# Performance work log

Measured on AMD Instinct MI355X. Metric: run time of the kernel, lower is better.

Reference implementation:

```python
import jax, jax.numpy as jnp
import numpy as np

B = 256
# (Cin, Cout, K, Hout) for each of the 6 deformable conv layers; input is 33x33
_LAYERS = [(1, 16, 3, 31), (16, 32, 3, 29), (32, 16, 5, 25), (16, 16, 7, 19), (16, 8, 5, 15), (8, 4, 3, 13)]


def setup_inputs() -> dict:
    key = jax.random.key(0)
    ks = jax.random.split(key, 24)
    inp = {"x": jax.random.normal(ks[0], (B, 1, 33, 33), dtype=jnp.float32)}
    for i, (ci, co, k, ho) in enumerate(_LAYERS):
        inp[f"off{i+1}"] = jax.random.normal(ks[1 + i], (1, 2 * k * k, ho, ho), dtype=jnp.float32)
        inp[f"w{i+1}"] = jax.random.normal(ks[7 + i], (co, ci, k, k), dtype=jnp.float32) / float(np.sqrt(ci * k * k))
        inp[f"b{i+1}"] = jnp.zeros((co,), jnp.float32)
    inp["w7"] = jax.random.normal(ks[13], (13 * 13 * 4, 256), dtype=jnp.float32) / 26.0
    inp["b7"] = jnp.zeros((256,), jnp.float32)
    inp["w8"] = jax.random.normal(ks[14], (256, 10), dtype=jnp.float32) / 16.0
    inp["b8"] = jnp.zeros((10,), jnp.float32)
    inp["perm"] = jnp.arange(13 * 13, dtype=jnp.int32)  # fixed spatial permutation (perm_6.ordenar)
    return inp


def _deform_conv(x, offset, weight, bias):
    # torchvision DeformConv2d, stride=1, padding=0, fixed offsets shared across batch.
    Bn, Cin, H, W = x.shape
    Cout, _, K, _ = weight.shape
    Ho, Wo = offset.shape[-2], offset.shape[-1]
    K2 = K * K
    off = offset[0].reshape(K2, 2, Ho, Wo)  # channel layout: [2k]=dy, [2k+1]=dx
    ky, kx = jnp.meshgrid(jnp.arange(K), jnp.arange(K), indexing='ij')
    py = jnp.arange(Ho, dtype=x.dtype)[None, :, None] + ky.reshape(-1, 1, 1) + off[:, 0]  # [K2,Ho,Wo]
    px = jnp.arange(Wo, dtype=x.dtype)[None, None, :] + kx.reshape(-1, 1, 1) + off[:, 1]
    y0f = jnp.floor(py); x0f = jnp.floor(px)
    wy = py - y0f; wx = px - x0f
    y0 = y0f.astype(jnp.int32); x0 = x0f.astype(jnp.int32)
    xf = x.reshape(Bn, Cin, H * W)

    def gather(yi, xi):
        valid = ((yi >= 0) & (yi < H) & (xi >= 0) & (xi < W)).astype(x.dtype)
        idx = (jnp.clip(yi, 0, H - 1) * W + jnp.clip(xi, 0, W - 1)).reshape(-1)
        v = xf[:, :, idx].reshape(Bn, Cin, K2, Ho, Wo)
        return v * valid[None, None]

    s = (gather(y0, x0) * ((1 - wy) * (1 - wx))[None, None]
         + gather(y0, x0 + 1) * ((1 - wy) * wx)[None, None]
         + gather(y0 + 1, x0) * (wy * (1 - wx))[None, None]
         + gather(y0 + 1, x0 + 1) * (wy * wx)[None, None])  # [B,Cin,K2,Ho,Wo]
    out = jnp.einsum('bckhw,ock->bohw', s, weight.reshape(Cout, Cin, K2))
    return out + bias[None, :, None, None]


def reference(x, off1, off2, off3, off4, off5, off6,
              w1, b1, w2, b2, w3, b3, w4, b4, w5, b5, w6, b6,
              w7, b7, w8, b8, perm):
    offs = (off1, off2, off3, off4, off5, off6)
    ws = (w1, w2, w3, w4, w5, w6)
    bs = (b1, b2, b3, b4, b5, b6)
    for off, w, b in zip(offs, ws, bs):
        x = jax.nn.relu(_deform_conv(x, off, w, b))
    Bn = x.shape[0]
    x = x.reshape(Bn, 4, 13 * 13)[:, :, perm].reshape(Bn, -1)  # perm_6.ordenar as spatial permutation
    h = jax.nn.relu(x @ w7 + b7)
    return h @ w8 + b8
```

## Files before the change

### kernel.cpp

```cpp
#include <hip/hip_runtime.h>

template<int N> struct IC { static constexpr int val = N; };

struct WtArgs { const float* src[6]; int co[6], ci[6], k2[6], dstoff[6]; };

__global__ __launch_bounds__(256)
void transpose_weights(WtArgs a, float* __restrict__ dst0)
{
    const int L = blockIdx.x;
    const float* __restrict__ s = a.src[L];
    float* __restrict__ d = dst0 + a.dstoff[L];
    const int co = a.co[L], ci = a.ci[L], k2 = a.k2[L];
    const int n = co * ci * k2;
    for (int i = threadIdx.x; i < n; i += 256) {
        int k = i % k2;
        int c = (i / k2) % ci;
        int o = i / (k2 * ci);
        d[(k * ci + c) * co + o] = s[i];
    }
}

struct MetaArgs { const float* off[6]; int P[6], K[6], WO[6], H[6], W[6], base[6]; };

__global__ __launch_bounds__(256)
void build_meta(MetaArgs a, float* __restrict__ meta0)
{
    const int L = blockIdx.y;
    const float* __restrict__ off = a.off[L];
    const int P = a.P[L], K = a.K[L], WOv = a.WO[L], H = a.H[L], Wv = a.W[L];
    const int N = P * K * K;
    float* __restrict__ m = meta0 + (size_t)a.base[L] * 8;
    for (int e = blockIdx.x * 256 + threadIdx.x; e < N; e += gridDim.x * 256) {
        const int k = e / P, p = e - k * P;
        const int ho = p / WOv, wo = p - ho * WOv;
        const int ky = k / K, kx = k - ky * K;
        const float dy = off[(2 * k)     * P + p];
        const float dx = off[(2 * k + 1) * P + p];
        const float py = (float)(ho + ky) + dy;
        const float px = (float)(wo + kx) + dx;
        const float y0f = floorf(py), x0f = floorf(px);
        const float wy = py - y0f, wx = px - x0f;
        const int y0 = (int)y0f, x0 = (int)x0f;
        const int y1 = y0 + 1,  x1 = x0 + 1;
        const bool vy0 = ((unsigned)y0 < (unsigned)H);
        const bool vy1 = ((unsigned)y1 < (unsigned)H);
        const bool vx0 = ((unsigned)x0 < (unsigned)Wv);
        const bool vx1 = ((unsigned)x1 < (unsigned)Wv);
        const int cy0 = min(max(y0, 0), H - 1) * Wv;
        const int cy1 = min(max(y1, 0), H - 1) * Wv;
        const int cx0 = min(max(x0, 0), Wv - 1);
        const int cx1 = min(max(x1, 0), Wv - 1);
        int4 mi;
        mi.x = cy0 + cx0; mi.y = cy0 + cx1; mi.z = cy1 + cx0; mi.w = cy1 + cx1;
        float4 mw;
        mw.x = (vy0 && vx0) ? (1.f - wy) * (1.f - wx) : 0.f;
        mw.y = (vy0 && vx1) ? (1.f - wy) * wx         : 0.f;
        mw.z = (vy1 && vx0) ? wy * (1.f - wx)         : 0.f;
        mw.w = (vy1 && vx1) ? wy * wx                 : 0.f;
        *(int4*)(m + (size_t)e * 8)       = mi;
        *(float4*)(m + (size_t)e * 8 + 4) = mw;
    }
}

template<int CIN, int CINW, int COUT, int K, int H, int W, int HO, int WO,
         int S, int KSEG, int NT, int NCOMB, bool SPLITOUT, bool MET,
         int NSL = 1, int CINL = 0>
__global__ __launch_bounds__(NT)
void deform_lds(const float* __restrict__ x0, const float* __restrict__ x1,
                const float* __restrict__ x2, const float* __restrict__ off,
                const float* __restrict__ meta, const float* __restrict__ wT,
                const float* __restrict__ bias, float* __restrict__ y,
                size_t pstride)
{
    constexpr int K2 = K * K, HW = H * W, P = HO * WO;
    constexpr int PW = ((P + 63) / 64) * 64;
    constexpr int KLEN = (K2 + KSEG - 1) / KSEG;
    constexpr int PSTR = (COUT % 2 == 0) ? COUT + 1 : COUT;
    static_assert(NT >= KSEG * PW, "NT too small for KSEG*PW");

    __shared__ __align__(16) float simg[HW * S];
    __shared__ float part[(KSEG > 1) ? (KSEG - 1) * P * PSTR : 1];

    const int tid = threadIdx.x;
    const int b   = blockIdx.x;
    const int h   = SPLITOUT ? blockIdx.y : 0;

    const size_t xoff = (size_t)b * CINW * HW + (SPLITOUT ? (size_t)h * CIN * HW : 0);
    const float* xb  = x0 + xoff;
    const float* xb1 = (NCOMB >= 2) ? (x1 + xoff) : nullptr;
    const float* xb2 = (NCOMB == 3) ? (x2 + xoff) : nullptr;
    for (int i = tid; i < CIN * HW; i += NT) {
        int c = i / HW, hw = i - c * HW;
        bool ok = true;
        if constexpr (SPLITOUT) ok = (h * CIN + c < CINW);
        float v = 0.f;
        if (ok) {
            v = xb[i];
            if constexpr (NCOMB >= 2) v += xb1[i];
            if constexpr (NCOMB == 3) v += xb2[i];
            if constexpr (NCOMB >= 2) v = fmaxf(v, 0.f);
        }
        simg[hw * S + c] = v;
    }
    __syncthreads();

    const int g  = tid / PW;
    const int p  = tid - g * PW;
    const int pc = (p < P) ? p : (P - 1);
    const bool active = (p < P);

    float acc[COUT];
#pragma unroll
    for (int o = 0; o < COUT; ++o) acc[o] = 0.f;

    if (g < KSEG) {
        if (g == 0 && (!SPLITOUT || h == 0)) {
#pragma unroll
            for (int o = 0; o < COUT; ++o) acc[o] = bias[o];
        }
        const int ho = pc / WO, wo = pc - ho * WO;
        const int kb = g * KLEN;

        auto run = [&](auto nc4tag) {
            constexpr int NC4 = decltype(nc4tag)::val;

            auto fma_block = [&](int i00, int i01, int i10, int i11,
                                 float w00, float w01, float w10, float w11,
                                 int kku) {
                const float* __restrict__ r00 = simg + i00 * S;
                const float* __restrict__ r01 = simg + i01 * S;
                const float* __restrict__ r10 = simg + i10 * S;
                const float* __restrict__ r11 = simg + i11 * S;
                const float* __restrict__ wk = wT + kku * (CINW * COUT)
                                             + (SPLITOUT ? h * (CIN * COUT) : 0);
                if constexpr (CIN % 4 == 0) {
#pragma unroll
                    for (int c4 = 0; c4 < NC4; ++c4) {
                        const float4 v00 = *(const float4*)(r00 + c4 * 4);
                        const float4 v01 = *(const float4*)(r01 + c4 * 4);
                        const float4 v10 = *(const float4*)(r10 + c4 * 4);
                        const float4 v11 = *(const float4*)(r11 + c4 * 4);
                        float4 sa;
                        sa.x = fmaf(w00, v00.x, fmaf(w01, v01.x, fmaf(w10, v10.x, w11 * v11.x)));
                        sa.y = fmaf(w00, v00.y, fmaf(w01, v01.y, fmaf(w10, v10.y, w11 * v11.y)));
                        sa.z = fmaf(w00, v00.z, fmaf(w01, v01.z, fmaf(w10, v10.z, w11 * v11.z)));
                        sa.w = fmaf(w00, v00.w, fmaf(w01, v01.w, fmaf(w10, v10.w, w11 * v11.w)));
                        const float* __restrict__ wc = wk + (c4 * 4) * COUT;
#pragma unroll
                        for (int o = 0; o < COUT; ++o) acc[o] = fmaf(wc[o], sa.x, acc[o]);
#pragma unroll
                        for (int o = 0; o < COUT; ++o) acc[o] = fmaf(wc[COUT + o], sa.y, acc[o]);
#pragma unroll
                        for (int o = 0; o < COUT; ++o) acc[o] = fmaf(wc[2 * COUT + o], sa.z, acc[o]);
#pragma unroll
                        for (int o = 0; o < COUT; ++o) acc[o] = fmaf(wc[3 * COUT + o], sa.w, acc[o]);
                    }
                } else {
#pragma unroll
                    for (int c = 0; c < CIN; ++c) {
                        float sa = fmaf(w00, r00[c], fmaf(w01, r01[c],
                                   fmaf(w10, r10[c], w11 * r11[c])));
#pragma unroll
                        for (int o = 0; o < COUT; ++o)
                            acc[o] = fmaf(wk[c * COUT + o], sa, acc[o]);
                    }
                }
            };

            if constexpr (MET) {
                const int kf = (kb < K2) ? kb : (K2 - 1);
                int4   nmi = *(const int4*)  (meta + (size_t)(kf * P + pc) * 8);
                float4 nmw = *(const float4*)(meta + (size_t)(kf * P + pc) * 8 + 4);

#pragma unroll 1
                for (int j = 0; j < KLEN; ++j) {
                    const int k  = kb + j;
                    const int kk = (k < K2) ? k : (K2 - 1);
                    const int4   mi  = nmi;
                    const float4 mwv = nmw;
                    const int kn = (k + 1 < K2) ? (k + 1) : (K2 - 1);
                    nmi = *(const int4*)  (meta + (size_t)(kn * P + pc) * 8);
                    nmw = *(const float4*)(meta + (size_t)(kn * P + pc) * 8 + 4);

                    float w00 = mwv.x, w01 = mwv.y, w10 = mwv.z, w11 = mwv.w;
                    if constexpr (K2 % KSEG != 0) {
                        const float kv = (k < K2) ? 1.f : 0.f;
                        w00 *= kv; w01 *= kv; w10 *= kv; w11 *= kv;
                    }
                    const int kku = __builtin_amdgcn_readfirstlane(kk);
                    fma_block(mi.x, mi.y, mi.z, mi.w, w00, w01, w10, w11, kku);
                }
            } else {
                const int kf = (kb < K2) ? kb : (K2 - 1);
                float ndy = off[(2 * kf)     * P + pc];
                float ndx = off[(2 * kf + 1) * P + pc];

#pragma unroll 1
                for (int j = 0; j < KLEN; ++j) {
                    const int k  = kb + j;
                    const int kk = (k < K2) ? k : (K2 - 1);
                    const float dy = ndy, dx = ndx;
                    const int kn = (k + 1 < K2) ? (k + 1) : (K2 - 1);
                    ndy = off[(2 * kn)     * P + pc];
                    ndx = off[(2 * kn + 1) * P + pc];

                    const int ky = kk / K, kx = kk - ky * K;
                    const float py = (float)(ho + ky) + dy;
                    const float px = (float)(wo + kx) + dx;
                    const float y0f = floorf(py), x0f = floorf(px);
                    const float wy = py - y0f, wx = px - x0f;
                    const int y0 = (int)y0f, x0 = (int)x0f;
                    const int y1 = y0 + 1,  x1i = x0 + 1;
                    const bool vy0 = ((unsigned)y0  < (unsigned)H);
                    const bool vy1 = ((unsigned)y1  < (unsigned)H);
                    const bool vx0 = ((unsigned)x0  < (unsigned)W);
                    const bool vx1 = ((unsigned)x1i < (unsigned)W);
                    const int cy0 = min(max(y0, 0), H - 1) * W;
                    const int cy1 = min(max(y1, 0), H - 1) * W;
                    const int cx0 = min(max(x0, 0), W - 1);
                    const int cx1 = min(max(x1i, 0), W - 1);
                    float w00 = (vy0 && vx0) ? (1.f - wy) * (1.f - wx) : 0.f;
                    float w01 = (vy0 && vx1) ? (1.f - wy) * wx         : 0.f;
                    float w10 = (vy1 && vx0) ? wy * (1.f - wx)         : 0.f;
                    float w11 = (vy1 && vx1) ? wy * wx                 : 0.f;
                    if constexpr (K2 % KSEG != 0) {
                        const float kv = (k < K2) ? 1.f : 0.f;
                        w00 *= kv; w01 *= kv; w10 *= kv; w11 *= kv;
                    }
                    const int kku = __builtin_amdgcn_readfirstlane(kk);
                    fma_block(cy0 + cx0, cy0 + cx1, cy1 + cx0, cy1 + cx1,
                              w00, w01, w10, w11, kku);
                }
            }
        };

        if constexpr (SPLITOUT && CINL > 0) {
            if (h == NSL - 1) run(IC<(CINL + 3) / 4>{});
            else              run(IC<(CIN + 3) / 4>{});
        } else {
            run(IC<(CIN + 3) / 4>{});
        }

        if (g > 0 && active) {
#pragma unroll
            for (int o = 0; o < COUT; ++o)
                part[(g - 1) * (P * PSTR) + p * PSTR + o] = acc[o];
        }
    }

    if constexpr (KSEG > 1) __syncthreads();

    if (g == 0 && active) {
        if constexpr (KSEG > 1) {
#pragma unroll
            for (int gg = 1; gg < KSEG; ++gg)
#pragma unroll
                for (int o = 0; o < COUT; ++o)
                    acc[o] += part[(gg - 1) * (P * PSTR) + p * PSTR + o];
        }
        float* yb = y + (SPLITOUT ? (size_t)h * pstride : 0) + (size_t)b * COUT * P;
#pragma unroll
        for (int o = 0; o < COUT; ++o)
            yb[o * P + p] = SPLITOUT ? acc[o] : fmaxf(acc[o], 0.f);
    }
}

__global__ __launch_bounds__(256)
void fc_head(const float* __restrict__ x6, const float* __restrict__ w7,
             const float* __restrict__ b7, const float* __restrict__ w8,
             const float* __restrict__ b8, const int* __restrict__ perm,
             float* __restrict__ out)
{
    constexpr int F = 676;
    __shared__ float sx[F];
    __shared__ float sh[256];

    const int tid = threadIdx.x;
    const int b   = blockIdx.x;

    for (int i = tid; i < F; i += 256) {
        int c = i / 169, p = i - c * 169;
        sx[i] = x6[(size_t)b * F + c * 169 + perm[p]];
    }
    __syncthreads();

    float acc = b7[tid];
#pragma unroll 4
    for (int i = 0; i < F; ++i)
        acc = fmaf(sx[i], w7[i * 256 + tid], acc);
    sh[tid] = fmaxf(acc, 0.f);
    __syncthreads();

    if (tid < 10) {
        float a = b8[tid];
#pragma unroll 8
        for (int j = 0; j < 256; ++j)
            a = fmaf(sh[j], w8[j * 10 + tid], a);
        out[(size_t)b * 10 + tid] = a;
    }
}

extern "C" void kernel_launch(void* const* d_in, const int* in_sizes, int n_in,
                              void* d_out, int out_size, void* d_ws, size_t ws_size,
                              hipStream_t stream)
{
    const float* x    = (const float*)d_in[0];
    const float* off1 = (const float*)d_in[1];
    const float* w1   = (const float*)d_in[2];
    const float* b1   = (const float*)d_in[3];
    const float* off2 = (const float*)d_in[4];
    const float* w2   = (const float*)d_in[5];
    const float* b2   = (const float*)d_in[6];
    const float* off3 = (const float*)d_in[7];
    const float* w3   = (const float*)d_in[8];
    const float* b3   = (const float*)d_in[9];
    const float* off4 = (const float*)d_in[10];
    const float* w4   = (const float*)d_in[11];
    const float* b4   = (const float*)d_in[12];
    const float* off5 = (const float*)d_in[13];
    const float* w5   = (const float*)d_in[14];
    const float* b5   = (const float*)d_in[15];
    const float* off6 = (const float*)d_in[16];
    const float* w6   = (const float*)d_in[17];
    const float* b6   = (const float*)d_in[18];
    const float* w7   = (const float*)d_in[19];
    const float* b7   = (const float*)d_in[20];
    const float* w8   = (const float*)d_in[21];
    const float* b8   = (const float*)d_in[22];
    const int*   perm = (const int*)d_in[23];
    float* out = (float*)d_out;

    const int woff[6] = {0, 144, 4752, 17552, 30096, 33296};
    float* ws   = (float*)d_ws;
    float* wt   = ws;
    float* buf0 = ws + 33792;
    float* buf1 = buf0 + 3936256;

    float* a1   = buf0;
    float* a2   = buf1;
    float* p1L2 = ws + 13419520;
    float* a3   = buf0;
    float* p1L3 = ws + 10859520;
    float* a4p0 = buf1;
    float* a4p1 = buf1 + 1478656;
    float* a5   = buf0;
    float* a6   = buf1;
    float* meta = ws + 20308992;

    const int mbase[6] = {0, 8649, 16218, 31843, 49532, 55157};
    const int MTOT = 56678;

    const bool splitL3 = (ws_size >= (size_t)13419520 * sizeof(float));
    const bool splitL2 = (ws_size >= (size_t)20308992 * sizeof(float));
    const bool metaOK  = (ws_size >= (size_t)(20308992 + MTOT * 8) * sizeof(float));
    const bool split3  = (ws_size >= (size_t)24245248 * sizeof(float));
    const size_t X      = 10825728;
    const size_t pstrL2 = (size_t)(p1L2 - a2);
    const size_t pstrL4 = 1478656;

    WtArgs wa;
    wa.src[0] = w1; wa.src[1] = w2; wa.src[2] = w3;
    wa.src[3] = w4; wa.src[4] = w5; wa.src[5] = w6;
    const int cos[6] = {16, 32, 16, 16, 8, 4};
    const int cis[6] = {1, 16, 32, 16, 16, 8};
    const int k2s[6] = {9, 9, 25, 49, 25, 9};
    for (int i = 0; i < 6; ++i) {
        wa.co[i] = cos[i]; wa.ci[i] = cis[i];
        wa.k2[i] = k2s[i]; wa.dstoff[i] = woff[i];
    }
    transpose_weights<<<dim3(6), dim3(256), 0, stream>>>(wa, wt);

    const dim3 g1(256), g2(256, 2), g3(256, 3);

    if (metaOK) {
        MetaArgs ma;
        ma.off[0] = off1; ma.off[1] = off2; ma.off[2] = off3;
        ma.off[3] = off4; ma.off[4] = off5; ma.off[5] = off6;
        const int Ps[6]  = {961, 841, 625, 361, 225, 169};
        const int Ks[6]  = {3, 3, 5, 7, 5, 3};
        const int WOs[6] = {31, 29, 25, 19, 15, 13};
        const int Hs[6]  = {33, 31, 29, 25, 19, 15};
        const int Ws_[6] = {33, 31, 29, 25, 19, 15};
        for (int i = 0; i < 6; ++i) {
            ma.P[i] = Ps[i]; ma.K[i] = Ks[i]; ma.WO[i] = WOs[i];
            ma.H[i] = Hs[i]; ma.W[i] = Ws_[i]; ma.base[i] = mbase[i];
        }
        build_meta<<<dim3(64, 6), dim3(256), 0, stream>>>(ma, meta);

        deform_lds< 1,  1, 16, 3, 33, 33, 31, 31,  1, 1, 1024, 1, false, true>
            <<<g1, dim3(1024), 0, stream>>>(x, nullptr, nullptr, off1, meta + (size_t)mbase[0]*8, wt + woff[0], b1, a1, 0);
        deform_lds< 8, 16, 32, 3, 31, 31, 29, 29, 12, 1,  896, 1, true,  true>
            <<<g2, dim3(896),  0, stream>>>(a1, nullptr, nullptr, off2, meta + (size_t)mbase[1]*8, wt + woff[1], b2, a2, pstrL2);

        if (split3) {
            deform_lds<12, 32, 16, 5, 29, 29, 25, 25, 12, 1,  640, 2, true,  true, 3, 8>
                <<<g3, dim3(640),  0, stream>>>(a2, p1L2, nullptr, off3, meta + (size_t)mbase[2]*8, wt + woff[2], b3, a3, X);
            deform_lds< 8, 16, 16, 7, 25, 25, 19, 19, 12, 2,  768, 3, true,  true>
                <<<g2, dim3(768),  0, stream>>>(a3, a3 + X, a3 + 2 * X, off4, meta + (size_t)mbase[3]*8, wt + woff[3], b4, a4p0, pstrL4);
        } else {
            deform_lds<16, 32, 16, 5, 29, 29, 25, 25, 20, 1,  640, 2, true,  true>
                <<<g2, dim3(640),  0, stream>>>(a2, p1L2, nullptr, off3, meta + (size_t)mbase[2]*8, wt + woff[2], b3, a3, X);
            deform_lds< 8, 16, 16, 7, 25, 25, 19, 19, 12, 2,  768, 2, true,  true>
                <<<g2, dim3(768),  0, stream>>>(a3, a3 + X, nullptr, off4, meta + (size_t)mbase[3]*8, wt + woff[3], b4, a4p0, pstrL4);
        }

        deform_lds<16, 16,  8, 5, 19, 19, 15, 15, 20, 4, 1024, 2, false, true>
            <<<g1, dim3(1024), 0, stream>>>(a4p0, a4p1, nullptr, off5, meta + (size_t)mbase[4]*8, wt + woff[4], b5, a5, 0);
        deform_lds< 8,  8,  4, 3, 15, 15, 13, 13, 12, 5,  960, 1, false, true>
            <<<g1, dim3(960),  0, stream>>>(a5, nullptr, nullptr, off6, meta + (size_t)mbase[5]*8, wt + woff[5], b6, a6, 0);
    } else {
        deform_lds< 1,  1, 16, 3, 33, 33, 31, 31,  1, 1, 1024, 1, false, false>
            <<<g1, dim3(1024), 0, stream>>>(x, nullptr, nullptr, off1, nullptr, wt + woff[0], b1, a1, 0);
        if (splitL2) {
            deform_lds< 8, 16, 32, 3, 31, 31, 29, 29, 12, 1, 1024, 1, true, false>
                <<<g2, dim3(1024), 0, stream>>>(a1, nullptr, nullptr, off2, nullptr, wt + woff[1], b2, a2, pstrL2);
        } else {
            deform_lds<16, 16, 32, 3, 31, 31, 29, 29, 20, 1, 1024, 1, false, false>
                <<<g1, dim3(1024), 0, stream>>>(a1, nullptr, nullptr, off2, nullptr, wt + woff[1], b2, a2, 0);
        }
        if (splitL3) {
            if (splitL2) {
                deform_lds<16, 32, 16, 5, 29, 29, 25, 25, 20, 1, 1024, 2, true, false>
                    <<<g2, dim3(1024), 0, stream>>>(a2, p1L2, nullptr, off3, nullptr, wt + woff[2], b3, a3, X);
            } else {
                deform_lds<16, 32, 16, 5, 29, 29, 25, 25, 20, 1, 1024, 1, true, false>
                    <<<g2, dim3(1024), 0, stream>>>(a2, nullptr, nullptr, off3, nullptr, wt + woff[2], b3, a3, X);
            }
            deform_lds< 8, 16, 16, 7, 25, 25, 19, 19, 12, 2,  768, 2, true, false>
                <<<g2, dim3(768),  0, stream>>>(a3, a3 + X, nullptr, off4, nullptr, wt + woff[3], b4, a4p0, pstrL4);
        } else {
            deform_lds<32, 32, 16, 5, 29, 29, 25, 25, 36, 1, 1024, 1, false, false>
                <<<g1, dim3(1024), 0, stream>>>(a2, nullptr, nullptr, off3, nullptr, wt + woff[2], b3, a3, 0);
            deform_lds< 8, 16, 16, 7, 25, 25, 19, 19, 12, 2,  768, 1, true, false>
                <<<g2, dim3(768),  0, stream>>>(a3, nullptr, nullptr, off4, nullptr, wt + woff[3], b4, a4p0, pstrL4);
        }
        deform_lds<16, 16,  8, 5, 19, 19, 15, 15, 20, 4, 1024, 2, false, false>
            <<<g1, dim3(1024), 0, stream>>>(a4p0, a4p1, nullptr, off5, nullptr, wt + woff[4], b5, a5, 0);
        deform_lds< 8,  8,  4, 3, 15, 15, 13, 13, 12, 5,  960, 1, false, false>
            <<<g1, dim3(960),  0, stream>>>(a5, nullptr, nullptr, off6, nullptr, wt + woff[5], b6, a6, 0);
    }

    fc_head<<<dim3(256), dim3(256), 0, stream>>>(a6, w7, b7, w8, b8, perm, out);
}
```

Before: 256.5 us.

## Split layer-4 kernel taps across blocks and use four-way ILP in FC head

Layer 4 now splits its 49 kernel taps across two extra grid slices (KSPL=2) on top of the two channel halves. That gives a 256x4 grid of 384-thread blocks with no intra-block KSEG reduction. Layer 5 then sums four partial buffers when it loads its input. The FC head's serial dot-product chain is broken into four independent accumulators to raise instruction-level parallelism. The trade-off is more partial-sum traffic through global memory and a smaller per-block workload in exchange for more blocks in flight.

```diff
diff --git a/kernel.cpp b/kernel.cpp
--- a/kernel.cpp
+++ b/kernel.cpp
@@ -64,17 +64,18 @@
 
 template<int CIN, int CINW, int COUT, int K, int H, int W, int HO, int WO,
          int S, int KSEG, int NT, int NCOMB, bool SPLITOUT, bool MET,
-         int NSL = 1, int CINL = 0>
+         int NSL = 1, int CINL = 0, int NCHS = 1, int KSPL = 1>
 __global__ __launch_bounds__(NT)
 void deform_lds(const float* __restrict__ x0, const float* __restrict__ x1,
-                const float* __restrict__ x2, const float* __restrict__ off,
-                const float* __restrict__ meta, const float* __restrict__ wT,
-                const float* __restrict__ bias, float* __restrict__ y,
-                size_t pstride)
+                const float* __restrict__ x2, const float* __restrict__ x3,
+                const float* __restrict__ off, const float* __restrict__ meta,
+                const float* __restrict__ wT, const float* __restrict__ bias,
+                float* __restrict__ y, size_t pstride)
 {
     constexpr int K2 = K * K, HW = H * W, P = HO * WO;
     constexpr int PW = ((P + 63) / 64) * 64;
-    constexpr int KLEN = (K2 + KSEG - 1) / KSEG;
+    constexpr int K2B  = (K2 + KSPL - 1) / KSPL;
+    constexpr int KLEN = (K2B + KSEG - 1) / KSEG;
     constexpr int PSTR = (COUT % 2 == 0) ? COUT + 1 : COUT;
     static_assert(NT >= KSEG * PW, "NT too small for KSEG*PW");
 
@@ -83,21 +84,25 @@
 
     const int tid = threadIdx.x;
     const int b   = blockIdx.x;
-    const int h   = SPLITOUT ? blockIdx.y : 0;
-
-    const size_t xoff = (size_t)b * CINW * HW + (SPLITOUT ? (size_t)h * CIN * HW : 0);
+    const int hy  = SPLITOUT ? blockIdx.y : 0;
+    const int hch = (KSPL > 1) ? (hy % NCHS) : hy;
+    const int hk  = (KSPL > 1) ? (hy / NCHS) : 0;
+
+    const size_t xoff = (size_t)b * CINW * HW + (SPLITOUT ? (size_t)hch * CIN * HW : 0);
     const float* xb  = x0 + xoff;
     const float* xb1 = (NCOMB >= 2) ? (x1 + xoff) : nullptr;
-    const float* xb2 = (NCOMB == 3) ? (x2 + xoff) : nullptr;
+    const float* xb2 = (NCOMB >= 3) ? (x2 + xoff) : nullptr;
+    const float* xb3 = (NCOMB >= 4) ? (x3 + xoff) : nullptr;
     for (int i = tid; i < CIN * HW; i += NT) {
         int c = i / HW, hw = i - c * HW;
         bool ok = true;
-        if constexpr (SPLITOUT) ok = (h * CIN + c < CINW);
+        if constexpr (SPLITOUT) ok = (hch * CIN + c < CINW);
         float v = 0.f;
         if (ok) {
             v = xb[i];
             if constexpr (NCOMB >= 2) v += xb1[i];
-            if constexpr (NCOMB == 3) v += xb2[i];
+            if constexpr (NCOMB >= 3) v += xb2[i];
+            if constexpr (NCOMB >= 4) v += xb3[i];
             if constexpr (NCOMB >= 2) v = fmaxf(v, 0.f);
         }
         simg[hw * S + c] = v;
@@ -114,12 +119,13 @@
     for (int o = 0; o < COUT; ++o) acc[o] = 0.f;
 
     if (g < KSEG) {
-        if (g == 0 && (!SPLITOUT || h == 0)) {
+        if ((!SPLITOUT || hy == 0) && g == 0) {
 #pragma unroll
             for (int o = 0; o < COUT; ++o) acc[o] = bias[o];
         }
         const int ho = pc / WO, wo = pc - ho * WO;
-        const int kb = g * KLEN;
+        const int kb   = hk * K2B + g * KLEN;
+        const int kend = (KSPL > 1) ? min(K2, hk * K2B + K2B) : K2;
 
         auto run = [&](auto nc4tag) {
             constexpr int NC4 = decltype(nc4tag)::val;
@@ -132,7 +138,7 @@
                 const float* __restrict__ r10 = simg + i10 * S;
                 const float* __restrict__ r11 = simg + i11 * S;
                 const float* __restrict__ wk = wT + kku * (CINW * COUT)
-                                             + (SPLITOUT ? h * (CIN * COUT) : 0);
+                                             + (SPLITOUT ? hch * (CIN * COUT) : 0);
                 if constexpr (CIN % 4 == 0) {
 #pragma unroll
                     for (int c4 = 0; c4 < NC4; ++c4) {
@@ -183,8 +189,8 @@
                     nmw = *(const float4*)(meta + (size_t)(kn * P + pc) * 8 + 4);
 
                     float w00 = mwv.x, w01 = mwv.y, w10 = mwv.z, w11 = mwv.w;
-                    if constexpr (K2 % KSEG != 0) {
-                        const float kv = (k < K2) ? 1.f : 0.f;
+                    if constexpr (K2 % (KSEG * KSPL) != 0) {
+                        const float kv = (k < kend) ? 1.f : 0.f;
                         w00 *= kv; w01 *= kv; w10 *= kv; w11 *= kv;
                     }
                     const int kku = __builtin_amdgcn_readfirstlane(kk);
@@ -223,8 +229,8 @@
                     float w01 = (vy0 && vx1) ? (1.f - wy) * wx         : 0.f;
                     float w10 = (vy1 && vx0) ? wy * (1.f - wx)         : 0.f;
                     float w11 = (vy1 && vx1) ? wy * wx                 : 0.f;
-                    if constexpr (K2 % KSEG != 0) {
-                        const float kv = (k < K2) ? 1.f : 0.f;
+                    if constexpr (K2 % (KSEG * KSPL) != 0) {
+                        const float kv = (k < kend) ? 1.f : 0.f;
                         w00 *= kv; w01 *= kv; w10 *= kv; w11 *= kv;
                     }
                     const int kku = __builtin_amdgcn_readfirstlane(kk);
@@ -235,8 +241,8 @@
         };
 
         if constexpr (SPLITOUT && CINL > 0) {
-            if (h == NSL - 1) run(IC<(CINL + 3) / 4>{});
-            else              run(IC<(CIN + 3) / 4>{});
+            if (hch == NSL - 1) run(IC<(CINL + 3) / 4>{});
+            else                run(IC<(CIN + 3) / 4>{});
         } else {
             run(IC<(CIN + 3) / 4>{});
         }
@@ -258,7 +264,7 @@
                 for (int o = 0; o < COUT; ++o)
                     acc[o] += part[(gg - 1) * (P * PSTR) + p * PSTR + o];
         }
-        float* yb = y + (SPLITOUT ? (size_t)h * pstride : 0) + (size_t)b * COUT * P;
+        float* yb = y + (SPLITOUT ? (size_t)hy * pstride : 0) + (size_t)b * COUT * P;
 #pragma unroll
         for (int o = 0; o < COUT; ++o)
             yb[o * P + p] = SPLITOUT ? acc[o] : fmaxf(acc[o], 0.f);
@@ -284,11 +290,15 @@
     }
     __syncthreads();
 
-    float acc = b7[tid];
-#pragma unroll 4
-    for (int i = 0; i < F; ++i)
-        acc = fmaf(sx[i], w7[i * 256 + tid], acc);
-    sh[tid] = fmaxf(acc, 0.f);
+    float a0 = 0.f, a1 = 0.f, a2 = 0.f, a3 = 0.f;
+#pragma unroll 2
+    for (int i = 0; i < 169; ++i) {
+        a0 = fmaf(sx[i],       w7[(size_t)i * 256 + tid],         a0);
+        a1 = fmaf(sx[169 + i], w7[(size_t)(169 + i) * 256 + tid], a1);
+        a2 = fmaf(sx[338 + i], w7[(size_t)(338 + i) * 256 + tid], a2);
+        a3 = fmaf(sx[507 + i], w7[(size_t)(507 + i) * 256 + tid], a3);
+    }
+    sh[tid] = fmaxf(b7[tid] + ((a0 + a1) + (a2 + a3)), 0.f);
     __syncthreads();
 
     if (tid < 10) {
@@ -342,7 +352,6 @@
     float* a3   = buf0;
     float* p1L3 = ws + 10859520;
     float* a4p0 = buf1;
-    float* a4p1 = buf1 + 1478656;
     float* a5   = buf0;
     float* a6   = buf1;
     float* meta = ws + 20308992;
@@ -370,7 +379,7 @@
     }
     transpose_weights<<<dim3(6), dim3(256), 0, stream>>>(wa, wt);
 
-    const dim3 g1(256), g2(256, 2), g3(256, 3);
+    const dim3 g1(256), g2(256, 2), g3(256, 3), g4(256, 4);
 
     if (metaOK) {
         MetaArgs ma;
@@ -388,56 +397,58 @@
         build_meta<<<dim3(64, 6), dim3(256), 0, stream>>>(ma, meta);
 
         deform_lds< 1,  1, 16, 3, 33, 33, 31, 31,  1, 1, 1024, 1, false, true>
-            <<<g1, dim3(1024), 0, stream>>>(x, nullptr, nullptr, off1, meta + (size_t)mbase[0]*8, wt + woff[0], b1, a1, 0);
+            <<<g1, dim3(1024), 0, stream>>>(x, nullptr, nullptr, nullptr, off1, meta + (size_t)mbase[0]*8, wt + woff[0], b1, a1, 0);
         deform_lds< 8, 16, 32, 3, 31, 31, 29, 29, 12, 1,  896, 1, true,  true>
-            <<<g2, dim3(896),  0, stream>>>(a1, nullptr, nullptr, off2, meta + (size_t)mbase[1]*8, wt + woff[1], b2, a2, pstrL2);
+            <<<g2, dim3(896),  0, stream>>>(a1, nullptr, nullptr, nullptr, off2, meta + (size_t)mbase[1]*8, wt + woff[1], b2, a2, pstrL2);
 
         if (split3) {
             deform_lds<12, 32, 16, 5, 29, 29, 25, 25, 12, 1,  640, 2, true,  true, 3, 8>
-                <<<g3, dim3(640),  0, stream>>>(a2, p1L2, nullptr, off3, meta + (size_t)mbase[2]*8, wt + woff[2], b3, a3, X);
-            deform_lds< 8, 16, 16, 7, 25, 25, 19, 19, 12, 2,  768, 3, true,  true>
-                <<<g2, dim3(768),  0, stream>>>(a3, a3 + X, a3 + 2 * X, off4, meta + (size_t)mbase[3]*8, wt + woff[3], b4, a4p0, pstrL4);
+                <<<g3, dim3(640),  0, stream>>>(a2, p1L2, nullptr, nullptr, off3, meta + (size_t)mbase[2]*8, wt + woff[2], b3, a3, X);
+            deform_lds< 8, 16, 16, 7, 25, 25, 19, 19, 12, 1,  384, 3, true,  true, 1, 0, 2, 2>
+                <<<g4, dim3(384),  0, stream>>>(a3, a3 + X, a3 + 2 * X, nullptr, off4, meta + (size_t)mbase[3]*8, wt + woff[3], b4, a4p0, pstrL4);
+            deform_lds<16, 16,  8, 5, 19, 19, 15, 15, 20, 4, 1024, 4, false, true>
+                <<<g1, dim3(1024), 0, stream>>>(a4p0, a4p0 + pstrL4, a4p0 + 2 * pstrL4, a4p0 + 3 * pstrL4, off5, meta + (size_t)mbase[4]*8, wt + woff[4], b5, a5, 0);
         } else {
             deform_lds<16, 32, 16, 5, 29, 29, 25, 25, 20, 1,  640, 2, true,  true>
-                <<<g2, dim3(640),  0, stream>>>(a2, p1L2, nullptr, off3, meta + (size_t)mbase[2]*8, wt + woff[2], b3, a3, X);
+                <<<g2, dim3(640),  0, stream>>>(a2, p1L2, nullptr, nullptr, off3, meta + (size_t)mbase[2]*8, wt + woff[2], b3, a3, X);
             deform_lds< 8, 16, 16, 7, 25, 25, 19, 19, 12, 2,  768, 2, true,  true>
-                <<<g2, dim3(768),  0, stream>>>(a3, a3 + X, nullptr, off4, meta + (size_t)mbase[3]*8, wt + woff[3], b4, a4p0, pstrL4);
-        }
-
-        deform_lds<16, 16,  8, 5, 19, 19, 15, 15, 20, 4, 1024, 2, false, true>
-            <<<g1, dim3(1024), 0, stream>>>(a4p0, a4p1, nullptr, off5, meta + (size_t)mbase[4]*8, wt + woff[4], b5, a5, 0);
+                <<<g2, dim3(768),  0, stream>>>(a3, a3 + X, nullptr, nullptr, off4, meta + (size_t)mbase[3]*8, wt + woff[3], b4, a4p0, pstrL4);
+            deform_lds<16, 16,  8, 5, 19, 19, 15, 15, 20, 4, 1024, 2, false, true>
+                <<<g1, dim3(1024), 0, stream>>>(a4p0, a4p0 + pstrL4, nullptr, nullptr, off5, meta + (size_t)mbase[4]*8, wt + woff[4], b5, a5, 0);
+        }
+
         deform_lds< 8,  8,  4, 3, 15, 15, 13, 13, 12, 5,  960, 1, false, true>
-            <<<g1, dim3(960),  0, stream>>>(a5, nullptr, nullptr, off6, meta + (size_t)mbase[5]*8, wt + woff[5], b6, a6, 0);
+            <<<g1, dim3(960),  0, stream>>>(a5, nullptr, nullptr, nullptr, off6, meta + (size_t)mbase[5]*8, wt + woff[5], b6, a6, 0);
     } else {
         deform_lds< 1,  1, 16, 3, 33, 33, 31, 31,  1, 1, 1024, 1, false, false>
-            <<<g1, dim3(1024), 0, stream>>>(x, nullptr, nullptr, off1, nullptr, wt + woff[0], b1, a1, 0);
+            <<<g1, dim3(1024), 0, stream>>>(x, nullptr, nullptr, nullptr, off1, nullptr, wt + woff[0], b1, a1, 0);
         if (splitL2) {
             deform_lds< 8, 16, 32, 3, 31, 31, 29, 29, 12, 1, 1024, 1, true, false>
-                <<<g2, dim3(1024), 0, stream>>>(a1, nullptr, nullptr, off2, nullptr, wt + woff[1], b2, a2, pstrL2);
+                <<<g2, dim3(1024), 0, stream>>>(a1, nullptr, nullptr, nullptr, off2, nullptr, wt + woff[1], b2, a2, pstrL2);
         } else {
             deform_lds<16, 16, 32, 3, 31, 31, 29, 29, 20, 1, 1024, 1, false, false>
-                <<<g1, dim3(1024), 0, stream>>>(a1, nullptr, nullptr, off2, nullptr, wt + woff[1], b2, a2, 0);
+                <<<g1, dim3(1024), 0, stream>>>(a1, nullptr, nullptr, nullptr, off2, nullptr, wt + woff[1], b2, a2, 0);
         }
         if (splitL3) {
             if (splitL2) {
                 deform_lds<16, 32, 16, 5, 29, 29, 25, 25, 20, 1, 1024, 2, true, false>
-                    <<<g2, dim3(1024), 0, stream>>>(a2, p1L2, nullptr, off3, nullptr, wt + woff[2], b3, a3, X);
+                    <<<g2, dim3(1024), 0, stream>>>(a2, p1L2, nullptr, nullptr, off3, nullptr, wt + woff[2], b3, a3, X);
             } else {
                 deform_lds<16, 32, 16, 5, 29, 29, 25, 25, 20, 1, 1024, 1, true, false>
-                    <<<g2, dim3(1024), 0, stream>>>(a2, nullptr, nullptr, off3, nullptr, wt + woff[2], b3, a3, X);
+                    <<<g2, dim3(1024), 0, stream>>>(a2, nullptr, nullptr, nullptr, off3, nullptr, wt + woff[2], b3, a3, X);
             }
             deform_lds< 8, 16, 16, 7, 25, 25, 19, 19, 12, 2,  768, 2, true, false>
-                <<<g2, dim3(768),  0, stream>>>(a3, a3 + X, nullptr, off4, nullptr, wt + woff[3], b4, a4p0, pstrL4);
+                <<<g2, dim3(768),  0, stream>>>(a3, a3 + X, nullptr, nullptr, off4, nullptr, wt + woff[3], b4, a4p0, pstrL4);
         } else {
             deform_lds<32, 32, 16, 5, 29, 29, 25, 25, 36, 1, 1024, 1, false, false>
-                <<<g1, dim3(1024), 0, stream>>>(a2, nullptr, nullptr, off3, nullptr, wt + woff[2], b3, a3, 0);
+                <<<g1, dim3(1024), 0, stream>>>(a2, nullptr, nullptr, nullptr, off3, nullptr, wt + woff[2], b3, a3, 0);
             deform_lds< 8, 16, 16, 7, 25, 25, 19, 19, 12, 2,  768, 1, true, false>
-                <<<g2, dim3(768),  0, stream>>>(a3, nullptr, nullptr, off4, nullptr, wt + woff[3], b4, a4p0, pstrL4);
+                <<<g2, dim3(768),  0, stream>>>(a3, nullptr, nullptr, nullptr, off4, nullptr, wt + woff[3], b4, a4p0, pstrL4);
         }
         deform_lds<16, 16,  8, 5, 19, 19, 15, 15, 20, 4, 1024, 2, false, false>
-            <<<g1, dim3(1024), 0, stream>>>(a4p0, a4p1, nullptr, off5, nullptr, wt + woff[4], b5, a5, 0);
+            <<<g1, dim3(1024), 0, stream>>>(a4p0, a4p0 + pstrL4, nullptr, nullptr, off5, nullptr, wt + woff[4], b5, a5, 0);
         deform_lds< 8,  8,  4, 3, 15, 15, 13, 13, 12, 5,  960, 1, false, false>
-            <<<g1, dim3(960),  0, stream>>>(a5, nullptr, nullptr, off6, nullptr, wt + woff[5], b6, a6, 0);
+            <<<g1, dim3(960),  0, stream>>>(a5, nullptr, nullptr, nullptr, off6, nullptr, wt + woff[5], b6, a6, 0);
     }
 
     fc_head<<<dim3(256), dim3(256), 0, stream>>>(a6, w7, b7, w8, b8, perm, out);
```

Result: slower. 280.2 us (+9.3%).
